# Kernel tuning notes

Measured on AMD Instinct MI355X. Metric: run time of the kernel, lower is better.

## Reference

```python
import jax, jax.numpy as jnp
import numpy as np

# Module config (init_kwargs)
RESOLUTION = 512   # output canvas H = W
PATCH_SIZE = 64    # ps
NUM_PATCHES = 512  # K
BATCH = 16         # B


def setup_inputs() -> dict:
    key = jax.random.key(0)
    k1, k2 = jax.random.split(key)
    patch_logits = jax.random.normal(
        k1, (BATCH, NUM_PATCHES, 1, PATCH_SIZE, PATCH_SIZE), dtype=jnp.float32)
    # top-left (h, w) coords, in-bounds like PatchSampler would emit
    coords = jax.random.randint(
        k2, (BATCH, NUM_PATCHES, 2), 0, RESOLUTION - PATCH_SIZE + 1, dtype=jnp.int64
        if jax.config.jax_enable_x64 else jnp.int32)
    return {"patch_logits": patch_logits, "coords": coords}


def reference(patch_logits, coords):
    """Faithful jax version of PatchICL_Level.aggregate (no prev_pred).

    patch_logits: [B, K, 1, ps, ps] float
    coords:       [B, K, 2] int (h, w) top-left corners
    returns:      [B, 1, H, W] scatter-added patches normalized by overlap counts.
    """
    B, K, _, ps, _ = patch_logits.shape
    H = W = RESOLUTION
    ar = jnp.arange(ps)
    # per-pixel absolute indices, [B, K, ps, ps]
    hh = coords[:, :, 0, None, None] + ar[None, None, :, None]
    ww = coords[:, :, 1, None, None] + ar[None, None, None, :]
    hh = jnp.broadcast_to(hh, (B, K, ps, ps))
    ww = jnp.broadcast_to(ww, (B, K, ps, ps))
    bb = jnp.broadcast_to(jnp.arange(B)[:, None, None, None], (B, K, ps, ps))
    vals = patch_logits[:, :, 0]  # [B, K, ps, ps]
    # scatter-add patches and counts; out-of-bounds indices are dropped,
    # matching the original code's boundary clipping of patch extents.
    output = jnp.zeros((B, H, W), dtype=patch_logits.dtype)
    output = output.at[bb, hh, ww].add(vals, mode='drop')
    counts = jnp.zeros((B, H, W), dtype=patch_logits.dtype)
    counts = counts.at[bb, hh, ww].add(jnp.ones_like(vals), mode='drop')
    aggregated = output / jnp.maximum(counts, 1.0)  # counts.clamp(min=1)
    return aggregated[:, None]  # [B, 1, H, W]
```

## Files before the change

kernel.cpp:

```cpp
#include <hip/hip_runtime.h>

#define RES 512
#define PS 64
#define NPATCH 512
#define BATCH 16
#define NTILE 8
#define NLISTS (BATCH * NTILE * NTILE)
#define LIST_CAP 512

__global__ void bin_kernel(const int* __restrict__ coords,
                           int* __restrict__ cnt,
                           unsigned* __restrict__ lists) {
    int p = blockIdx.x * blockDim.x + threadIdx.x;
    if (p >= BATCH * NPATCH) return;
    int b = p >> 9;
    int k = p & (NPATCH - 1);
    int ch = coords[2 * p + 0];
    int cw = coords[2 * p + 1];
    unsigned pack = (unsigned)k | ((unsigned)ch << 10) | ((unsigned)cw << 19);
    int tr0 = ch >> 6, tr1 = (ch + PS - 1) >> 6;
    int tc0 = cw >> 6, tc1 = (cw + PS - 1) >> 6;
    for (int tr = tr0; tr <= tr1; ++tr) {
        for (int tc = tc0; tc <= tc1; ++tc) {
            int list = b * (NTILE * NTILE) + tr * NTILE + tc;
            int idx = atomicAdd(&cnt[list], 1);
            lists[list * LIST_CAP + idx] = pack;
        }
    }
}

__global__ __launch_bounds__(256) void gather_kernel(
        const float* __restrict__ logits,
        const int* __restrict__ cnt,
        const unsigned* __restrict__ lists,
        float* __restrict__ out) {
    __shared__ unsigned sl[LIST_CAP];
    __shared__ int s_m;

    int blk  = blockIdx.x;
    int band = blk & 3;
    int list = blk >> 2;
    int b  = list >> 6;
    int tr = (list >> 3) & 7;
    int tc = list & 7;
    int R0 = tr * 64 + band * 16;

    if (threadIdx.x == 0) s_m = 0;
    __syncthreads();

    int n = cnt[list];
    for (int i = threadIdx.x; i < n; i += 256) {
        unsigned e = lists[list * LIST_CAP + i];
        int ch = (e >> 10) & 511;
        if (ch <= R0 + 15 && ch + 63 >= R0)
            sl[atomicAdd(&s_m, 1)] = e;
    }
    __syncthreads();
    int m = s_m;

    int lane = threadIdx.x & 63;
    int w    = threadIdx.x >> 6;
    int gcol = tc * 64 + lane;
    int row0 = R0 + w * 4;

    float sum0 = 0.f, sum1 = 0.f, sum2 = 0.f, sum3 = 0.f;
    float cc0  = 0.f, cc1  = 0.f, cc2  = 0.f, cc3  = 0.f;

#pragma unroll 4
    for (int i = 0; i < m; ++i) {
        unsigned e = __builtin_amdgcn_readfirstlane(sl[i]);
        int k  = e & 1023;
        int ch = (e >> 10) & 511;
        int cw = (e >> 19) & 511;

        int dc = gcol - cw;
        float colw = ((unsigned)dc < 64u) ? 1.0f : 0.0f;
        int dcc = min(max(dc, 0), 63);

        int dr0 = row0 - ch;
        const float* p = logits + ((size_t)(b * NPATCH + k) << 12) + dcc;

        int r0 = min(max(dr0 + 0, 0), 63);
        int r1 = min(max(dr0 + 1, 0), 63);
        int r2 = min(max(dr0 + 2, 0), 63);
        int r3 = min(max(dr0 + 3, 0), 63);
        float v0 = p[r0 << 6];
        float v1 = p[r1 << 6];
        float v2 = p[r2 << 6];
        float v3 = p[r3 << 6];
        float w0 = ((unsigned)(dr0 + 0) < 64u) ? colw : 0.0f;
        float w1 = ((unsigned)(dr0 + 1) < 64u) ? colw : 0.0f;
        float w2 = ((unsigned)(dr0 + 2) < 64u) ? colw : 0.0f;
        float w3 = ((unsigned)(dr0 + 3) < 64u) ? colw : 0.0f;
        sum0 += v0 * w0;  cc0 += w0;
        sum1 += v1 * w1;  cc1 += w1;
        sum2 += v2 * w2;  cc2 += w2;
        sum3 += v3 * w3;  cc3 += w3;
    }

    size_t obase = ((size_t)b * RES + row0) * RES + gcol;
    __builtin_nontemporal_store(sum0 / fmaxf(cc0, 1.0f), &out[obase + 0 * RES]);
    __builtin_nontemporal_store(sum1 / fmaxf(cc1, 1.0f), &out[obase + 1 * RES]);
    __builtin_nontemporal_store(sum2 / fmaxf(cc2, 1.0f), &out[obase + 2 * RES]);
    __builtin_nontemporal_store(sum3 / fmaxf(cc3, 1.0f), &out[obase + 3 * RES]);
}

extern "C" void kernel_launch(void* const* d_in, const int* in_sizes, int n_in,
                              void* d_out, int out_size, void* d_ws, size_t ws_size,
                              hipStream_t stream) {
    const float* logits = (const float*)d_in[0];
    const int*   coords = (const int*)d_in[1];
    float* out = (float*)d_out;

    int*      cnt   = (int*)d_ws;
    unsigned* lists = (unsigned*)((char*)d_ws + 4096);

    hipMemsetAsync(cnt, 0, NLISTS * sizeof(int), stream);
    bin_kernel<<<(BATCH * NPATCH + 255) / 256, 256, 0, stream>>>(coords, cnt, lists);
    gather_kernel<<<NLISTS * 4, 256, 0, stream>>>(logits, cnt, lists, out);
}
```

Measured before the change: 219.7 us.

## Fuse patch binning into gather kernel, scanning coords per block

Removes the memset and the separate binning kernel. Each gather block now reads all coordinates for its batch item and filters the patches that overlap its row band and column tile into shared memory. This drops two launches and the global list traffic, at the cost of every block scanning 512 coordinate pairs. The main loop unroll factor is also raised from 4 to 8.

```diff
diff --git a/kernel.cpp b/kernel.cpp
--- a/kernel.cpp
+++ b/kernel.cpp
@@ -5,36 +5,12 @@
 #define NPATCH 512
 #define BATCH 16
 #define NTILE 8
-#define NLISTS (BATCH * NTILE * NTILE)
-#define LIST_CAP 512
 
-__global__ void bin_kernel(const int* __restrict__ coords,
-                           int* __restrict__ cnt,
-                           unsigned* __restrict__ lists) {
-    int p = blockIdx.x * blockDim.x + threadIdx.x;
-    if (p >= BATCH * NPATCH) return;
-    int b = p >> 9;
-    int k = p & (NPATCH - 1);
-    int ch = coords[2 * p + 0];
-    int cw = coords[2 * p + 1];
-    unsigned pack = (unsigned)k | ((unsigned)ch << 10) | ((unsigned)cw << 19);
-    int tr0 = ch >> 6, tr1 = (ch + PS - 1) >> 6;
-    int tc0 = cw >> 6, tc1 = (cw + PS - 1) >> 6;
-    for (int tr = tr0; tr <= tr1; ++tr) {
-        for (int tc = tc0; tc <= tc1; ++tc) {
-            int list = b * (NTILE * NTILE) + tr * NTILE + tc;
-            int idx = atomicAdd(&cnt[list], 1);
-            lists[list * LIST_CAP + idx] = pack;
-        }
-    }
-}
-
-__global__ __launch_bounds__(256) void gather_kernel(
+__global__ __launch_bounds__(256) void fused_gather_kernel(
         const float* __restrict__ logits,
-        const int* __restrict__ cnt,
-        const unsigned* __restrict__ lists,
+        const int*   __restrict__ coords,
         float* __restrict__ out) {
-    __shared__ unsigned sl[LIST_CAP];
+    __shared__ unsigned sl[NPATCH];
     __shared__ int s_m;
 
     int blk  = blockIdx.x;
@@ -44,29 +20,32 @@
     int tr = (list >> 3) & 7;
     int tc = list & 7;
     int R0 = tr * 64 + band * 16;
+    int C0 = tc * 64;
 
     if (threadIdx.x == 0) s_m = 0;
     __syncthreads();
 
-    int n = cnt[list];
-    for (int i = threadIdx.x; i < n; i += 256) {
-        unsigned e = lists[list * LIST_CAP + i];
-        int ch = (e >> 10) & 511;
-        if (ch <= R0 + 15 && ch + 63 >= R0)
-            sl[atomicAdd(&s_m, 1)] = e;
+    const int2* cb = (const int2*)(coords + (size_t)b * NPATCH * 2);
+    for (int k = threadIdx.x; k < NPATCH; k += 256) {
+        int2 c = cb[k];
+        int ch = c.x, cw = c.y;
+        if (ch <= R0 + 15 && ch >= R0 - 63 && cw <= C0 + 63 && cw >= C0 - 63) {
+            unsigned pack = (unsigned)k | ((unsigned)ch << 10) | ((unsigned)cw << 19);
+            sl[atomicAdd(&s_m, 1)] = pack;
+        }
     }
     __syncthreads();
     int m = s_m;
 
     int lane = threadIdx.x & 63;
     int w    = threadIdx.x >> 6;
-    int gcol = tc * 64 + lane;
+    int gcol = C0 + lane;
     int row0 = R0 + w * 4;
 
     float sum0 = 0.f, sum1 = 0.f, sum2 = 0.f, sum3 = 0.f;
     float cc0  = 0.f, cc1  = 0.f, cc2  = 0.f, cc3  = 0.f;
 
-#pragma unroll 4
+#pragma unroll 8
     for (int i = 0; i < m; ++i) {
         unsigned e = __builtin_amdgcn_readfirstlane(sl[i]);
         int k  = e & 1023;
@@ -111,11 +90,7 @@
     const float* logits = (const float*)d_in[0];
     const int*   coords = (const int*)d_in[1];
     float* out = (float*)d_out;
+    (void)d_ws; (void)ws_size;
 
-    int*      cnt   = (int*)d_ws;
-    unsigned* lists = (unsigned*)((char*)d_ws + 4096);
-
-    hipMemsetAsync(cnt, 0, NLISTS * sizeof(int), stream);
-    bin_kernel<<<(BATCH * NPATCH + 255) / 256, 256, 0, stream>>>(coords, cnt, lists);
-    gather_kernel<<<NLISTS * 4, 256, 0, stream>>>(logits, cnt, lists, out);
+    fused_gather_kernel<<<BATCH * NTILE * NTILE * 4, 256, 0, stream>>>(logits, coords, out);
 }
```

Measured after the change: 210.5 us. 1.04x faster.
